# Performance work log

Hardware: AMD Instinct MI355X
Metric: run time of the kernel (lower is better)

## Reference

```python
import jax, jax.numpy as jnp
import numpy as np
from jax import lax

B, P, MAXDIM, RES = 128, 2048, 3, 4096
H = 1024          # hidden_dim
F = 256           # ph_feature_dim
H4 = H // 4       # 256
H2 = H // 2       # 512
LN_EPS = 1e-5


def setup_inputs() -> dict:
    key = jax.random.key(0)
    ks = jax.random.split(key, 16)
    inp = {
        "pd": jax.random.normal(ks[0], (B, P, 3), dtype=jnp.float32),
        "pd_lengths": jax.random.randint(ks[1], (B,), 0, P, dtype=jnp.int32),
        "betti_numbers": jax.random.randint(ks[2], (B, MAXDIM), 0, 12, dtype=jnp.int32),
        "persistence_images": jax.random.normal(ks[3], (B, RES), dtype=jnp.float32),
        # pd_encoder: Linear(3,F) -> LayerNorm(F) -> GELU -> Linear(F,H4)
        "W1": jax.random.normal(ks[4], (3, F), dtype=jnp.float32) * 0.1,
        "b1": jnp.zeros((F,), dtype=jnp.float32),
        "ln_g": jnp.ones((F,), dtype=jnp.float32),
        "ln_b": jnp.zeros((F,), dtype=jnp.float32),
        "W2": jax.random.normal(ks[5], (F, H4), dtype=jnp.float32) * 0.06,
        "b2": jnp.zeros((H4,), dtype=jnp.float32),
        # Embedding(10, H4)
        "betti_table": jax.random.normal(ks[6], (10, H4), dtype=jnp.float32),
        # Conv1d(1, H2, k=5, stride=2, pad=2)
        "conv_w": jax.random.normal(ks[7], (H2, 1, 5), dtype=jnp.float32) * 0.4,
        "conv_b": jnp.zeros((H2,), dtype=jnp.float32),
        # output_proj: Linear(H, H)
        "Wo": jax.random.normal(ks[8], (H, H), dtype=jnp.float32) * 0.03,
        "bo": jnp.zeros((H,), dtype=jnp.float32),
    }
    return inp


def reference(pd, pd_lengths, betti_numbers, persistence_images,
              W1, b1, ln_g, ln_b, W2, b2, betti_table, conv_w, conv_b, Wo, bo):
    dt = pd.dtype
    # --- PD branch: batched padded encode + masked mean pool ---
    mask = (jnp.arange(pd.shape[1])[None, :] < pd_lengths[:, None]).astype(dt)  # [B,P]
    h = jnp.einsum('bpi,if->bpf', pd, W1) + b1                                  # [B,P,F]
    mu = jnp.mean(h, axis=-1, keepdims=True)
    var = jnp.mean(jnp.square(h - mu), axis=-1, keepdims=True)                  # biased var (torch LN)
    h = (h - mu) * lax.rsqrt(var + LN_EPS) * ln_g + ln_b
    h = jax.nn.gelu(h, approximate=False)                                       # exact GELU (torch default)
    h = jnp.einsum('bpf,fd->bpd', h, W2) + b2                                   # [B,P,H4]
    counts = jnp.sum(mask, axis=1)                                              # [B]
    sums = jnp.einsum('bpd,bp->bd', h, mask)                                    # [B,H4]
    pd_pooled = jnp.where(counts[:, None] > 0, sums / jnp.maximum(counts, 1.0)[:, None], 0.0)
    # --- Betti branch: clamp -> embed -> mean over dims ---
    betti_feat = betti_table[jnp.clip(betti_numbers, 0, 9)].mean(axis=1)        # [B,H4]
    # --- Persistence-image branch: Conv1d(1,H2,k=5,s=2,p=2) then mean over positions ---
    pi = lax.conv_general_dilated(persistence_images[:, None, :], conv_w,
                                  window_strides=(2,), padding=[(2, 2)])        # [B,H2,L]
    pi_feat = pi.mean(axis=-1) + conv_b[None, :]                                # [B,H2]
    # --- Combine + output projection ---
    combined = jnp.concatenate([pd_pooled, betti_feat, pi_feat], axis=-1)       # [B,H]
    out = combined @ Wo + bo                                                    # [B,H]
    return out[:, None, :]                                                      # [B,1,H]
```

## Files before the change

kernel.cpp:

```cpp
#include <hip/hip_runtime.h>
#include <math.h>

constexpr int kB   = 128;
constexpr int kP   = 2048;
constexpr int kRES = 4096;
constexpr int kF   = 256;
constexpr int kH   = 1024;
constexpr float kLN_EPS = 1e-5f;
constexpr int kBN = 32;
constexpr int kBK = 64;
constexpr int kRSTD_BLOCKS = 512;

#if __has_builtin(__builtin_amdgcn_exp2f)
#define EXP2F __builtin_amdgcn_exp2f
#else
#define EXP2F exp2f
#endif
#if __has_builtin(__builtin_amdgcn_rcpf)
#define RCPF __builtin_amdgcn_rcpf
#else
#define RCPF(x) (1.0f / (x))
#endif

__device__ __forceinline__ float gelu_fast(float y) {
    const float a = fabsf(y);
    const float t = RCPF(fmaf(0.33267096f, a, 1.0f));
    const float e = EXP2F(-0.72134752f * y * y);
    const float p = fmaf(fmaf(0.37392780f, t, -0.04793990f), t, 0.17401210f);
    const float w = (p * t) * e;
    return fmaf(-a, w, fmaf(0.5f, y, 0.5f * a));
}

__device__ __forceinline__ void build_chain_starts(
    const int* __restrict__ plen, int C, int K, int tid,
    unsigned* s1, unsigned* s2, int* cs)
{
    if (tid < kB) s1[tid] = (unsigned)plen[tid] + (unsigned)K;
    __syncthreads();
    unsigned* src = s1; unsigned* dst = s2;
    #pragma unroll
    for (int d = 1; d < kB; d <<= 1) {
        if (tid < kB) dst[tid] = src[tid] + ((tid >= d) ? src[tid - d] : 0u);
        __syncthreads();
        unsigned* t = src; src = dst; dst = t;
    }
    const unsigned total = src[kB - 1];
    if (tid <= kB) {
        const unsigned pre = (tid == 0) ? 0u : src[tid - 1];
        cs[tid] = (int)(((unsigned long long)pre * (unsigned)C) / total);
    }
    __syncthreads();
}

__device__ __forceinline__ void ln_constants(
    const float* __restrict__ W1, const float* __restrict__ b1,
    int tid, float pr[14][4], float* cl)
{
    const float w0 = W1[tid], w1 = W1[256 + tid], w2 = W1[512 + tid], bb = b1[tid];
    float v[14] = { w0, w1, w2, bb, w0*w0, w0*w1, w0*w2, w1*w1, w1*w2, w2*w2,
                    w0*bb, w1*bb, w2*bb, bb*bb };
    #pragma unroll
    for (int off = 32; off; off >>= 1) {
        #pragma unroll
        for (int i = 0; i < 14; ++i) v[i] += __shfl_xor(v[i], off);
    }
    if ((tid & 63) == 0) {
        #pragma unroll
        for (int i = 0; i < 14; ++i) pr[i][tid >> 6] = v[i];
    }
    __syncthreads();
    if (tid < 14)
        cl[tid] = (pr[tid][0] + pr[tid][1] + pr[tid][2] + pr[tid][3]) * (1.f / 256.f);
    __syncthreads();
}

__global__ __launch_bounds__(256) void k0_setup(
    const int* __restrict__ plen, const float* __restrict__ W1,
    const float* __restrict__ b1, const float* __restrict__ ln_g,
    const float* __restrict__ pd,
    float* __restrict__ Wp, float* __restrict__ bp,
    int* __restrict__ cs_g, int4* __restrict__ ctab,
    float* __restrict__ rstdb, int C, int K)
{
    __shared__ unsigned s1[kB], s2[kB];
    __shared__ int cs[kB + 1];
    __shared__ float pr[14][4];
    __shared__ float cl[14];
    const int tid = threadIdx.x;
    const int bid = blockIdx.x;
    const int NB_TAB = C >> 8;

    if (bid >= NB_TAB) {
        ln_constants(W1, b1, tid, pr, cl);
        const float S0 = cl[0], S1c = cl[1], S2c = cl[2], Sb = cl[3];
        const float P00 = cl[4], P01 = cl[5], P02 = cl[6];
        const float P11 = cl[7], P12 = cl[8], P22 = cl[9];
        const float Q0 = cl[10], Q1 = cl[11], Q2 = cl[12], Rc = cl[13];
        const int rbase = (bid - NB_TAB) * 512;
        #pragma unroll
        for (int u = 0; u < 2; ++u) {
            const int r = rbase + u * 256 + tid;
            const float* rp = pd + (size_t)r * 3;
            const float x0 = rp[0], x1 = rp[1], x2 = rp[2];
            const float mu = fmaf(x2, S2c, fmaf(x1, S1c, fmaf(x0, S0, Sb)));
            const float sx = fmaf(P01 * x0, x1, fmaf(P02 * x0, x2, fmaf(P12 * x1, x2,
                             fmaf(Q0, x0, fmaf(Q1, x1, Q2 * x2)))));
            const float e2 = fmaf(P00 * x0, x0, fmaf(P11 * x1, x1, fmaf(P22 * x2, x2,
                             fmaf(2.f, sx, Rc))));
            rstdb[r] = rsqrtf(fmaf(-mu, mu, e2) + kLN_EPS);
        }
        return;
    }

    build_chain_starts(plen, C, K, tid, s1, s2, cs);

    const int c = bid * 256 + tid;
    {
        int lo = 0, hi = kB;
        while (hi - lo > 1) { const int mid = (lo + hi) >> 1; if (cs[mid] <= c) lo = mid; else hi = mid; }
        const int b = lo;
        const int m = cs[b + 1] - cs[b];
        const int j = c - cs[b];
        const int len = plen[b];
        const int T  = (len + 3) >> 2;
        const int l4 = (int)(((long long)j * T) / m);
        const int h4 = (int)(((long long)(j + 1) * T) / m);
        const int start = min(l4 * 4, len);
        const int cnt   = max(0, min(h4 * 4, len) - start);
        ctab[c] = make_int4(b, start, cnt, 0);
    }

    if (bid == 0) {
        if (tid <= kB) cs_g[tid] = cs[tid];
        ln_constants(W1, b1, tid, pr, cl);
        const float g = ln_g[tid];
        Wp[tid]       = (W1[tid]       - cl[0]) * g;
        Wp[256 + tid] = (W1[256 + tid] - cl[1]) * g;
        Wp[512 + tid] = (W1[512 + tid] - cl[2]) * g;
        bp[tid]       = (b1[tid]       - cl[3]) * g;
    }
}

__global__ __launch_bounds__(256) void k1_pd_partial(
    const float* __restrict__ pd, const float* __restrict__ Wp,
    const float* __restrict__ bp, const float* __restrict__ ln_b,
    const int4* __restrict__ ctab, const float* __restrict__ rstdb,
    float* __restrict__ partial)
{
    const int tid = threadIdx.x, lane = tid & 63, wave = tid >> 6;
    const int c = blockIdx.x * 4 + wave;
    const int4 ci = ctab[c];
    const int b = ci.x, start = ci.y, cnt = ci.z;

    const float4 w0q = ((const float4*)Wp)[lane];
    const float4 w1q = ((const float4*)Wp)[64 + lane];
    const float4 w2q = ((const float4*)Wp)[128 + lane];
    const float4 bpq = ((const float4*)bp)[lane];
    const float4 beq = ((const float4*)ln_b)[lane];

    float a0 = 0.f, a1 = 0.f, a2 = 0.f, a3 = 0.f;

#define ROW(x0, x1, x2, rs)                                                      \
    {                                                                            \
        const float h0 = fmaf((x2), w2q.x, fmaf((x1), w1q.x, fmaf((x0), w0q.x, bpq.x))); \
        const float h1 = fmaf((x2), w2q.y, fmaf((x1), w1q.y, fmaf((x0), w0q.y, bpq.y))); \
        const float h2 = fmaf((x2), w2q.z, fmaf((x1), w1q.z, fmaf((x0), w0q.z, bpq.z))); \
        const float h3 = fmaf((x2), w2q.w, fmaf((x1), w1q.w, fmaf((x0), w0q.w, bpq.w))); \
        a0 += gelu_fast(fmaf(h0, (rs), beq.x));                                  \
        a1 += gelu_fast(fmaf(h1, (rs), beq.y));                                  \
        a2 += gelu_fast(fmaf(h2, (rs), beq.z));                                  \
        a3 += gelu_fast(fmaf(h3, (rs), beq.w));                                  \
    }

    const int nq  = cnt >> 2;
    const int rem = cnt & 3;
    const float4* qp = (const float4*)(pd + ((size_t)b * kP + start) * 3);
    const float4* rs4 = (const float4*)(rstdb + (size_t)b * kP + start);
    for (int it = 0; it < nq; ++it) {
        const float4 f0 = qp[0];
        const float4 f1 = qp[1];
        const float4 f2 = qp[2];
        const float4 rq = rs4[it];
        qp += 3;
        ROW(f0.x, f0.y, f0.z, rq.x);
        ROW(f0.w, f1.x, f1.y, rq.y);
        ROW(f1.z, f1.w, f2.x, rq.z);
        ROW(f2.y, f2.z, f2.w, rq.w);
    }
    const float* rp = (const float*)qp;
    const float* rsp = rstdb + (size_t)b * kP + start + nq * 4;
    for (int it = 0; it < rem; ++it, rp += 3) {
        ROW(rp[0], rp[1], rp[2], rsp[it]);
    }
#undef ROW

    ((float4*)(partial + ((size_t)c << 8)))[lane] = make_float4(a0, a1, a2, a3);
}

__global__ __launch_bounds__(256) void k2_combined(
    const float* __restrict__ partial, const int* __restrict__ plen,
    const float* __restrict__ W2, const float* __restrict__ b2,
    const int* __restrict__ betti, const float* __restrict__ betti_table,
    const float* __restrict__ pimg, const float* __restrict__ conv_w,
    const float* __restrict__ conv_b, float* __restrict__ combined,
    const int* __restrict__ cs_g)
{
    __shared__ float red[4 * 256];
    __shared__ float ml[256];
    __shared__ float sred[2][4];
    const int b    = blockIdx.x;
    const int tid  = threadIdx.x;
    const int wave = tid >> 6;
    const int lane = tid & 63;

    if (blockIdx.y == 0) {
        const int len = plen[b];
        const int c0 = cs_g[b], c1 = cs_g[b + 1];

        float4 aq = make_float4(0.f, 0.f, 0.f, 0.f);
        float4 bq = make_float4(0.f, 0.f, 0.f, 0.f);
        int c = c0 + wave;
        for (; c + 4 < c1; c += 8) {
            const float4 v0 = ((const float4*)(partial + ((size_t)c << 8)))[lane];
            const float4 v1 = ((const float4*)(partial + ((size_t)(c + 4) << 8)))[lane];
            aq.x += v0.x; aq.y += v0.y; aq.z += v0.z; aq.w += v0.w;
            bq.x += v1.x; bq.y += v1.y; bq.z += v1.z; bq.w += v1.w;
        }
        if (c < c1) {
            const float4 v0 = ((const float4*)(partial + ((size_t)c << 8)))[lane];
            aq.x += v0.x; aq.y += v0.y; aq.z += v0.z; aq.w += v0.w;
        }
        aq.x += bq.x; aq.y += bq.y; aq.z += bq.z; aq.w += bq.w;
        ((float4*)red)[wave * 64 + lane] = aq;
        __syncthreads();
        const float inv = (len > 0) ? (1.f / (float)len) : 0.f;
        ml[tid] = (red[tid] + red[256 + tid] + red[512 + tid] + red[768 + tid]) * inv;
        __syncthreads();

        const float4* W24 = (const float4*)W2;
        float4 acc = make_float4(0.f, 0.f, 0.f, 0.f);
        const int f0 = wave * 64;
        #pragma unroll 8
        for (int i = 0; i < 64; ++i) {
            const float mv = ml[f0 + i];
            const float4 wv = W24[(size_t)(f0 + i) * 64 + lane];
            acc.x = fmaf(mv, wv.x, acc.x); acc.y = fmaf(mv, wv.y, acc.y);
            acc.z = fmaf(mv, wv.z, acc.z); acc.w = fmaf(mv, wv.w, acc.w);
        }
        ((float4*)red)[wave * 64 + lane] = acc;
        __syncthreads();
        const float o = (red[tid] + red[256 + tid]) + (red[512 + tid] + red[768 + tid]);
        combined[(size_t)b * kH + tid] = (len > 0) ? (o + b2[tid]) : 0.f;

        const int i0 = min(max(betti[b * 3 + 0], 0), 9);
        const int i1 = min(max(betti[b * 3 + 1], 0), 9);
        const int i2 = min(max(betti[b * 3 + 2], 0), 9);
        combined[(size_t)b * kH + 256 + tid] =
            (betti_table[i0 * 256 + tid] + betti_table[i1 * 256 + tid] +
             betti_table[i2 * 256 + tid]) * (1.f / 3.f);
    } else {
        const float4* x4 = (const float4*)(pimg + (size_t)b * kRES);
        float se = 0.f, so = 0.f;
        #pragma unroll
        for (int j = 0; j < 4; ++j) {
            const float4 v = x4[tid + j * 256];
            se += v.x + v.z;
            so += v.y + v.w;
        }
        #pragma unroll
        for (int off = 32; off; off >>= 1) {
            se += __shfl_xor(se, off);
            so += __shfl_xor(so, off);
        }
        if (lane == 0) { sred[0][wave] = se; sred[1][wave] = so; }
        __syncthreads();
        se = (sred[0][0] + sred[0][1]) + (sred[0][2] + sred[0][3]);
        so = (sred[1][0] + sred[1][1]) + (sred[1][2] + sred[1][3]);

        const float x0 = pimg[(size_t)b * kRES + 0];
        const float xe = pimg[(size_t)b * kRES + 4094];
        const float xo = pimg[(size_t)b * kRES + 4095];
        #pragma unroll
        for (int u = 0; u < 2; ++u) {
            const int cc = tid + u * 256;
            const float* w = conv_w + (size_t)cc * 5;
            const float v = w[0] * (se - xe) + w[1] * (so - xo) + w[2] * se +
                            w[3] * so + w[4] * (se - x0);
            combined[(size_t)b * kH + 512 + cc] = v * (1.f / 2048.f) + conv_b[cc];
        }
    }
}

__global__ __launch_bounds__(256) void k3a_outproj(
    const float* __restrict__ combined, const float* __restrict__ Wo,
    float* __restrict__ kpart, int KT)
{
    const int nt  = blockIdx.x;
    const int kt  = blockIdx.y;
    const int tid = threadIdx.x;
    const int n0  = nt * kBN;
    const int kchunk = kH / KT;
    const int nsub   = kchunk / kBK;

    __shared__ float At[kBK * 132];
    __shared__ float Bs[kBK * kBN];

    const int n8 = tid & 7;
    const int mg = tid >> 3;

    float4 acc0 = make_float4(0.f,0.f,0.f,0.f);
    float4 acc1 = make_float4(0.f,0.f,0.f,0.f);
    float4 acc2 = make_float4(0.f,0.f,0.f,0.f);
    float4 acc3 = make_float4(0.f,0.f,0.f,0.f);

    for (int sc = 0; sc < nsub; ++sc) {
        const int k0 = kt * kchunk + sc * kBK;
        __syncthreads();
        #pragma unroll
        for (int it = 0; it < 8; ++it) {
            const int idx = it * 256 + tid;
            const int m   = idx >> 4;
            const int c4  = idx & 15;
            const float4 v = *(const float4*)(combined + (size_t)m * kH + k0 + c4 * 4);
            At[(c4 * 4 + 0) * 132 + m] = v.x;
            At[(c4 * 4 + 1) * 132 + m] = v.y;
            At[(c4 * 4 + 2) * 132 + m] = v.z;
            At[(c4 * 4 + 3) * 132 + m] = v.w;
        }
        #pragma unroll
        for (int it = 0; it < 2; ++it) {
            const int idx = it * 256 + tid;
            const int kk  = idx >> 3;
            const int cc  = idx & 7;
            *(float4*)(Bs + kk * kBN + cc * 4) =
                *(const float4*)(Wo + (size_t)(k0 + kk) * kH + n0 + cc * 4);
        }
        __syncthreads();

        #pragma unroll 8
        for (int kk = 0; kk < kBK; ++kk) {
            const float4 av = *(const float4*)(At + kk * 132 + mg * 4);
            const float4 bv = *(const float4*)(Bs + kk * kBN + n8 * 4);
            acc0.x = fmaf(av.x, bv.x, acc0.x); acc0.y = fmaf(av.x, bv.y, acc0.y);
            acc0.z = fmaf(av.x, bv.z, acc0.z); acc0.w = fmaf(av.x, bv.w, acc0.w);
            acc1.x = fmaf(av.y, bv.x, acc1.x); acc1.y = fmaf(av.y, bv.y, acc1.y);
            acc1.z = fmaf(av.y, bv.z, acc1.z); acc1.w = fmaf(av.y, bv.w, acc1.w);
            acc2.x = fmaf(av.z, bv.x, acc2.x); acc2.y = fmaf(av.z, bv.y, acc2.y);
            acc2.z = fmaf(av.z, bv.z, acc2.z); acc2.w = fmaf(av.z, bv.w, acc2.w);
            acc3.x = fmaf(av.w, bv.x, acc3.x); acc3.y = fmaf(av.w, bv.y, acc3.y);
            acc3.z = fmaf(av.w, bv.z, acc3.z); acc3.w = fmaf(av.w, bv.w, acc3.w);
        }
    }

    float* base = kpart + ((size_t)kt * kB + mg * 4) * kH + n0 + n8 * 4;
    *(float4*)(base)          = acc0;
    *(float4*)(base + kH)     = acc1;
    *(float4*)(base + 2 * kH) = acc2;
    *(float4*)(base + 3 * kH) = acc3;
}

__global__ __launch_bounds__(256) void k3b_reduce(
    const float* __restrict__ kpart, const float* __restrict__ bo,
    float* __restrict__ out, int KT)
{
    const int g = blockIdx.x * 256 + threadIdx.x;
    const float4* kp = (const float4*)kpart;
    float4 a = make_float4(0.f, 0.f, 0.f, 0.f);
    float4 b = make_float4(0.f, 0.f, 0.f, 0.f);
    float4 cacc = make_float4(0.f, 0.f, 0.f, 0.f);
    float4 d = make_float4(0.f, 0.f, 0.f, 0.f);
    int t = 0;
    for (; t + 3 < KT; t += 4) {
        const float4 v0 = kp[(size_t)(t + 0) * (kB * kH / 4) + g];
        const float4 v1 = kp[(size_t)(t + 1) * (kB * kH / 4) + g];
        const float4 v2 = kp[(size_t)(t + 2) * (kB * kH / 4) + g];
        const float4 v3 = kp[(size_t)(t + 3) * (kB * kH / 4) + g];
        a.x += v0.x; a.y += v0.y; a.z += v0.z; a.w += v0.w;
        b.x += v1.x; b.y += v1.y; b.z += v1.z; b.w += v1.w;
        cacc.x += v2.x; cacc.y += v2.y; cacc.z += v2.z; cacc.w += v2.w;
        d.x += v3.x; d.y += v3.y; d.z += v3.z; d.w += v3.w;
    }
    for (; t < KT; ++t) {
        const float4 v0 = kp[(size_t)t * (kB * kH / 4) + g];
        a.x += v0.x; a.y += v0.y; a.z += v0.z; a.w += v0.w;
    }
    a.x += b.x + cacc.x + d.x;
    a.y += b.y + cacc.y + d.y;
    a.z += b.z + cacc.z + d.z;
    a.w += b.w + cacc.w + d.w;
    const float4 bq = ((const float4*)bo)[g & 255];
    a.x += bq.x; a.y += bq.y; a.z += bq.z; a.w += bq.w;
    ((float4*)out)[g] = a;
}

extern "C" void kernel_launch(void* const* d_in, const int* in_sizes, int n_in,
                              void* d_out, int out_size, void* d_ws, size_t ws_size,
                              hipStream_t stream) {
    const float* pd   = (const float*)d_in[0];
    const int*   plen = (const int*)  d_in[1];
    const int*   bnum = (const int*)  d_in[2];
    const float* pimg = (const float*)d_in[3];
    const float* W1   = (const float*)d_in[4];
    const float* b1   = (const float*)d_in[5];
    const float* lng  = (const float*)d_in[6];
    const float* lnb  = (const float*)d_in[7];
    const float* W2   = (const float*)d_in[8];
    const float* b2   = (const float*)d_in[9];
    const float* btab = (const float*)d_in[10];
    const float* cw   = (const float*)d_in[11];
    const float* cb   = (const float*)d_in[12];
    const float* Wo   = (const float*)d_in[13];
    const float* bo   = (const float*)d_in[14];
    float* out = (float*)d_out;

    int C = 2048;
    {
        const int Cs[3] = {8192, 4096, 2048};
        for (int i = 0; i < 3; ++i) {
            const size_t need = ((size_t)Cs[i] * 256 + (size_t)kB * kH + 768 + 256 + 132) * 4 +
                                (size_t)Cs[i] * 16 + (size_t)kB * kP * 4 + 256;
            if (ws_size >= need) { C = Cs[i]; break; }
        }
    }
    const int K  = (kB * kP + C - 129) / (C - 128);
    const int KT = C / 512;

    float* partial  = (float*)d_ws;
    float* combined = partial + (size_t)C * 256;
    float* Wp       = combined + (size_t)kB * kH;
    float* bpp      = Wp + 768;
    int*   cs_g     = (int*)(bpp + 256);
    int4*  ctab     = (int4*)(cs_g + 132);
    float* rstdb    = (float*)(ctab + C);
    float* kpart    = partial;

    k0_setup<<<dim3(C / 256 + kRSTD_BLOCKS), 256, 0, stream>>>(
        plen, W1, b1, lng, pd, Wp, bpp, cs_g, ctab, rstdb, C, K);
    k1_pd_partial<<<dim3(C / 4), 256, 0, stream>>>(pd, Wp, bpp, lnb, ctab, rstdb, partial);
    k2_combined<<<dim3(kB, 2), 256, 0, stream>>>(partial, plen, W2, b2, bnum, btab,
                                                 pimg, cw, cb, combined, cs_g);
    k3a_outproj<<<dim3(32, KT), 256, 0, stream>>>(combined, Wo, kpart, KT);
    k3b_reduce<<<dim3(kB), 256, 0, stream>>>(kpart, bo, out, KT);
}
```

Baseline: 52.38 us.

## Fuse setup kernel into PD partial kernel, recomputing chunk table and rstd inline

Removes the separate k0_setup launch. Every k1 block now recomputes the LayerNorm constants, chain starts and its chunk assignment, and each wave computes per-row rstd into shared memory instead of reading a precomputed global buffer. k2 also rebuilds the chain starts locally. This saves a launch plus the rstd and table round trips through global memory, at the cost of redundant per-block setup work (reductions and syncs) in every k1 and k2 block.

```diff
diff --git a/kernel.cpp b/kernel.cpp
--- a/kernel.cpp
+++ b/kernel.cpp
@@ -9,7 +9,6 @@
 constexpr float kLN_EPS = 1e-5f;
 constexpr int kBN = 32;
 constexpr int kBK = 64;
-constexpr int kRSTD_BLOCKS = 512;
 
 #if __has_builtin(__builtin_amdgcn_exp2f)
 #define EXP2F __builtin_amdgcn_exp2f
@@ -74,89 +73,54 @@
     __syncthreads();
 }
 
-__global__ __launch_bounds__(256) void k0_setup(
-    const int* __restrict__ plen, const float* __restrict__ W1,
-    const float* __restrict__ b1, const float* __restrict__ ln_g,
-    const float* __restrict__ pd,
-    float* __restrict__ Wp, float* __restrict__ bp,
-    int* __restrict__ cs_g, int4* __restrict__ ctab,
-    float* __restrict__ rstdb, int C, int K)
+__global__ __launch_bounds__(256) void k1_pd_partial(
+    const float* __restrict__ pd, const int* __restrict__ plen,
+    const float* __restrict__ W1, const float* __restrict__ b1,
+    const float* __restrict__ ln_g, const float* __restrict__ ln_b,
+    float* __restrict__ partial, int C, int K)
 {
     __shared__ unsigned s1[kB], s2[kB];
     __shared__ int cs[kB + 1];
     __shared__ float pr[14][4];
     __shared__ float cl[14];
-    const int tid = threadIdx.x;
-    const int bid = blockIdx.x;
-    const int NB_TAB = C >> 8;
-
-    if (bid >= NB_TAB) {
-        ln_constants(W1, b1, tid, pr, cl);
-        const float S0 = cl[0], S1c = cl[1], S2c = cl[2], Sb = cl[3];
-        const float P00 = cl[4], P01 = cl[5], P02 = cl[6];
-        const float P11 = cl[7], P12 = cl[8], P22 = cl[9];
-        const float Q0 = cl[10], Q1 = cl[11], Q2 = cl[12], Rc = cl[13];
-        const int rbase = (bid - NB_TAB) * 512;
-        #pragma unroll
-        for (int u = 0; u < 2; ++u) {
-            const int r = rbase + u * 256 + tid;
-            const float* rp = pd + (size_t)r * 3;
-            const float x0 = rp[0], x1 = rp[1], x2 = rp[2];
-            const float mu = fmaf(x2, S2c, fmaf(x1, S1c, fmaf(x0, S0, Sb)));
-            const float sx = fmaf(P01 * x0, x1, fmaf(P02 * x0, x2, fmaf(P12 * x1, x2,
-                             fmaf(Q0, x0, fmaf(Q1, x1, Q2 * x2)))));
-            const float e2 = fmaf(P00 * x0, x0, fmaf(P11 * x1, x1, fmaf(P22 * x2, x2,
-                             fmaf(2.f, sx, Rc))));
-            rstdb[r] = rsqrtf(fmaf(-mu, mu, e2) + kLN_EPS);
-        }
-        return;
-    }
-
+    __shared__ float rstd_s[4][64];
+    const int tid = threadIdx.x, lane = tid & 63, wave = tid >> 6;
+
+    ln_constants(W1, b1, tid, pr, cl);
     build_chain_starts(plen, C, K, tid, s1, s2, cs);
 
-    const int c = bid * 256 + tid;
-    {
-        int lo = 0, hi = kB;
-        while (hi - lo > 1) { const int mid = (lo + hi) >> 1; if (cs[mid] <= c) lo = mid; else hi = mid; }
-        const int b = lo;
-        const int m = cs[b + 1] - cs[b];
-        const int j = c - cs[b];
-        const int len = plen[b];
-        const int T  = (len + 3) >> 2;
-        const int l4 = (int)(((long long)j * T) / m);
-        const int h4 = (int)(((long long)(j + 1) * T) / m);
-        const int start = min(l4 * 4, len);
-        const int cnt   = max(0, min(h4 * 4, len) - start);
-        ctab[c] = make_int4(b, start, cnt, 0);
-    }
-
-    if (bid == 0) {
-        if (tid <= kB) cs_g[tid] = cs[tid];
-        ln_constants(W1, b1, tid, pr, cl);
-        const float g = ln_g[tid];
-        Wp[tid]       = (W1[tid]       - cl[0]) * g;
-        Wp[256 + tid] = (W1[256 + tid] - cl[1]) * g;
-        Wp[512 + tid] = (W1[512 + tid] - cl[2]) * g;
-        bp[tid]       = (b1[tid]       - cl[3]) * g;
-    }
-}
-
-__global__ __launch_bounds__(256) void k1_pd_partial(
-    const float* __restrict__ pd, const float* __restrict__ Wp,
-    const float* __restrict__ bp, const float* __restrict__ ln_b,
-    const int4* __restrict__ ctab, const float* __restrict__ rstdb,
-    float* __restrict__ partial)
-{
-    const int tid = threadIdx.x, lane = tid & 63, wave = tid >> 6;
+    const float S0 = cl[0], S1c = cl[1], S2c = cl[2], Sb = cl[3];
+    const float P00 = cl[4], P01 = cl[5], P02 = cl[6];
+    const float P11 = cl[7], P12 = cl[8], P22 = cl[9];
+    const float Q0 = cl[10], Q1 = cl[11], Q2 = cl[12], Rc = cl[13];
+
     const int c = blockIdx.x * 4 + wave;
-    const int4 ci = ctab[c];
-    const int b = ci.x, start = ci.y, cnt = ci.z;
-
-    const float4 w0q = ((const float4*)Wp)[lane];
-    const float4 w1q = ((const float4*)Wp)[64 + lane];
-    const float4 w2q = ((const float4*)Wp)[128 + lane];
-    const float4 bpq = ((const float4*)bp)[lane];
+    int lo = 0, hi = kB;
+    while (hi - lo > 1) { const int mid = (lo + hi) >> 1; if (cs[mid] <= c) lo = mid; else hi = mid; }
+    const int b = lo;
+    const int m = cs[b + 1] - cs[b];
+    const int j = c - cs[b];
+    const int len = plen[b];
+    const int T  = (len + 3) >> 2;
+    const int l4 = (int)(((long long)j * T) / m);
+    const int h4 = (int)(((long long)(j + 1) * T) / m);
+    const int start = min(l4 * 4, len);
+    const int cnt   = max(0, min(h4 * 4, len) - start);
+
+    const float4 W04 = ((const float4*)W1)[lane];
+    const float4 W14 = ((const float4*)W1)[64 + lane];
+    const float4 W24 = ((const float4*)W1)[128 + lane];
+    const float4 B14 = ((const float4*)b1)[lane];
+    const float4 G4  = ((const float4*)ln_g)[lane];
     const float4 beq = ((const float4*)ln_b)[lane];
+    const float4 w0q = make_float4((W04.x - S0) * G4.x, (W04.y - S0) * G4.y,
+                                   (W04.z - S0) * G4.z, (W04.w - S0) * G4.w);
+    const float4 w1q = make_float4((W14.x - S1c) * G4.x, (W14.y - S1c) * G4.y,
+                                   (W14.z - S1c) * G4.z, (W14.w - S1c) * G4.w);
+    const float4 w2q = make_float4((W24.x - S2c) * G4.x, (W24.y - S2c) * G4.y,
+                                   (W24.z - S2c) * G4.z, (W24.w - S2c) * G4.w);
+    const float4 bpq = make_float4((B14.x - Sb) * G4.x, (B14.y - Sb) * G4.y,
+                                   (B14.z - Sb) * G4.z, (B14.w - Sb) * G4.w);
 
     float a0 = 0.f, a1 = 0.f, a2 = 0.f, a3 = 0.f;
 
@@ -172,25 +136,39 @@
         a3 += gelu_fast(fmaf(h3, (rs), beq.w));                                  \
     }
 
-    const int nq  = cnt >> 2;
-    const int rem = cnt & 3;
-    const float4* qp = (const float4*)(pd + ((size_t)b * kP + start) * 3);
-    const float4* rs4 = (const float4*)(rstdb + (size_t)b * kP + start);
-    for (int it = 0; it < nq; ++it) {
-        const float4 f0 = qp[0];
-        const float4 f1 = qp[1];
-        const float4 f2 = qp[2];
-        const float4 rq = rs4[it];
-        qp += 3;
-        ROW(f0.x, f0.y, f0.z, rq.x);
-        ROW(f0.w, f1.x, f1.y, rq.y);
-        ROW(f1.z, f1.w, f2.x, rq.z);
-        ROW(f2.y, f2.z, f2.w, rq.w);
-    }
-    const float* rp = (const float*)qp;
-    const float* rsp = rstdb + (size_t)b * kP + start + nq * 4;
-    for (int it = 0; it < rem; ++it, rp += 3) {
-        ROW(rp[0], rp[1], rp[2], rsp[it]);
+    for (int off = 0; off < cnt; off += 64) {
+        const int n = min(64, cnt - off);
+        {
+            const int rr = start + off + ((lane < n) ? lane : 0);
+            const float* rp = pd + ((size_t)b * kP + rr) * 3;
+            const float x0 = rp[0], x1 = rp[1], x2 = rp[2];
+            const float mu = fmaf(x2, S2c, fmaf(x1, S1c, fmaf(x0, S0, Sb)));
+            const float sx = fmaf(P01 * x0, x1, fmaf(P02 * x0, x2, fmaf(P12 * x1, x2,
+                             fmaf(Q0, x0, fmaf(Q1, x1, Q2 * x2)))));
+            const float e2 = fmaf(P00 * x0, x0, fmaf(P11 * x1, x1, fmaf(P22 * x2, x2,
+                             fmaf(2.f, sx, Rc))));
+            rstd_s[wave][lane] = rsqrtf(fmaf(-mu, mu, e2) + kLN_EPS);
+        }
+        const int nq  = n >> 2;
+        const int rem = n & 3;
+        const float4* qp = (const float4*)(pd + ((size_t)b * kP + start + off) * 3);
+        for (int q = 0; q < nq; ++q) {
+            const float4 f0 = qp[0];
+            const float4 f1 = qp[1];
+            const float4 f2 = qp[2];
+            const float4 rq = *(const float4*)&rstd_s[wave][q * 4];
+            qp += 3;
+            ROW(f0.x, f0.y, f0.z, rq.x);
+            ROW(f0.w, f1.x, f1.y, rq.y);
+            ROW(f1.z, f1.w, f2.x, rq.z);
+            ROW(f2.y, f2.z, f2.w, rq.w);
+        }
+        if (rem) {
+            const float* rp = (const float*)qp;
+            for (int i = 0; i < rem; ++i, rp += 3) {
+                ROW(rp[0], rp[1], rp[2], rstd_s[wave][nq * 4 + i]);
+            }
+        }
     }
 #undef ROW
 
@@ -203,8 +181,10 @@
     const int* __restrict__ betti, const float* __restrict__ betti_table,
     const float* __restrict__ pimg, const float* __restrict__ conv_w,
     const float* __restrict__ conv_b, float* __restrict__ combined,
-    const int* __restrict__ cs_g)
-{
+    int C, int K)
+{
+    __shared__ unsigned s1[kB], s2[kB];
+    __shared__ int cs[kB + 1];
     __shared__ float red[4 * 256];
     __shared__ float ml[256];
     __shared__ float sred[2][4];
@@ -214,8 +194,9 @@
     const int lane = tid & 63;
 
     if (blockIdx.y == 0) {
+        build_chain_starts(plen, C, K, tid, s1, s2, cs);
         const int len = plen[b];
-        const int c0 = cs_g[b], c1 = cs_g[b + 1];
+        const int c0 = cs[b], c1 = cs[b + 1];
 
         float4 aq = make_float4(0.f, 0.f, 0.f, 0.f);
         float4 bq = make_float4(0.f, 0.f, 0.f, 0.f);
@@ -417,8 +398,7 @@
     {
         const int Cs[3] = {8192, 4096, 2048};
         for (int i = 0; i < 3; ++i) {
-            const size_t need = ((size_t)Cs[i] * 256 + (size_t)kB * kH + 768 + 256 + 132) * 4 +
-                                (size_t)Cs[i] * 16 + (size_t)kB * kP * 4 + 256;
+            const size_t need = ((size_t)Cs[i] * 256 + (size_t)kB * kH) * 4;
             if (ws_size >= need) { C = Cs[i]; break; }
         }
     }
@@ -427,18 +407,12 @@
 
     float* partial  = (float*)d_ws;
     float* combined = partial + (size_t)C * 256;
-    float* Wp       = combined + (size_t)kB * kH;
-    float* bpp      = Wp + 768;
-    int*   cs_g     = (int*)(bpp + 256);
-    int4*  ctab     = (int4*)(cs_g + 132);
-    float* rstdb    = (float*)(ctab + C);
     float* kpart    = partial;
 
-    k0_setup<<<dim3(C / 256 + kRSTD_BLOCKS), 256, 0, stream>>>(
-        plen, W1, b1, lng, pd, Wp, bpp, cs_g, ctab, rstdb, C, K);
-    k1_pd_partial<<<dim3(C / 4), 256, 0, stream>>>(pd, Wp, bpp, lnb, ctab, rstdb, partial);
+    k1_pd_partial<<<dim3(C / 4), 256, 0, stream>>>(pd, plen, W1, b1, lng, lnb,
+                                                   partial, C, K);
     k2_combined<<<dim3(kB, 2), 256, 0, stream>>>(partial, plen, W2, b2, bnum, btab,
-                                                 pimg, cw, cb, combined, cs_g);
+                                                 pimg, cw, cb, combined, C, K);
     k3a_outproj<<<dim3(32, KT), 256, 0, stream>>>(combined, Wo, kpart, KT);
     k3b_reduce<<<dim3(kB), 256, 0, stream>>>(kpart, bo, out, KT);
 }
```

Measured after the change: 53.71 us. 1.03x slower.

## Fuse output-projection split-K reduction into GEMM via atomic ticket counter

Applied to the files above, without the earlier changes.

Merges the split-K output projection and its reduction kernel into one launch. Each block takes an atomic ticket after writing its partial tile. The last 32 ticket holders spin until every block has finished, then each sums the partials for 4 output row groups and adds the bias. This removes one kernel launch and its gap, at the cost of a memset, a spin-wait that relies on all blocks being co-resident or already retired, and the reduction now running on only 32 blocks instead of 128.

```diff
diff --git a/kernel.cpp b/kernel.cpp
--- a/kernel.cpp
+++ b/kernel.cpp
@@ -291,9 +291,10 @@
     }
 }
 
-__global__ __launch_bounds__(256) void k3a_outproj(
+__global__ __launch_bounds__(256) void k3_fused(
     const float* __restrict__ combined, const float* __restrict__ Wo,
-    float* __restrict__ kpart, int KT)
+    float* __restrict__ kpart, const float* __restrict__ bo,
+    float* __restrict__ out, int* __restrict__ cnt3, int KT)
 {
     const int nt  = blockIdx.x;
     const int kt  = blockIdx.y;
@@ -304,6 +305,7 @@
 
     __shared__ float At[kBK * 132];
     __shared__ float Bs[kBK * kBN];
+    __shared__ int s_ticket;
 
     const int n8 = tid & 7;
     const int mg = tid >> 3;
@@ -357,40 +359,56 @@
     *(float4*)(base + kH)     = acc1;
     *(float4*)(base + 2 * kH) = acc2;
     *(float4*)(base + 3 * kH) = acc3;
-}
-
-__global__ __launch_bounds__(256) void k3b_reduce(
-    const float* __restrict__ kpart, const float* __restrict__ bo,
-    float* __restrict__ out, int KT)
-{
-    const int g = blockIdx.x * 256 + threadIdx.x;
+
+    __syncthreads();
+    if (tid == 0) {
+        __threadfence();
+        s_ticket = atomicAdd(cnt3, 1);
+    }
+    __syncthreads();
+    const int NB3 = 32 * KT;
+    const int ticket = s_ticket;
+    if (ticket < NB3 - 32) return;
+
+    if (tid == 0) {
+        while (__hip_atomic_load(cnt3, __ATOMIC_ACQUIRE, __HIP_MEMORY_SCOPE_AGENT) < NB3)
+            __builtin_amdgcn_s_sleep(8);
+    }
+    __syncthreads();
+    __threadfence();
+
     const float4* kp = (const float4*)kpart;
-    float4 a = make_float4(0.f, 0.f, 0.f, 0.f);
-    float4 b = make_float4(0.f, 0.f, 0.f, 0.f);
-    float4 cacc = make_float4(0.f, 0.f, 0.f, 0.f);
-    float4 d = make_float4(0.f, 0.f, 0.f, 0.f);
-    int t = 0;
-    for (; t + 3 < KT; t += 4) {
-        const float4 v0 = kp[(size_t)(t + 0) * (kB * kH / 4) + g];
-        const float4 v1 = kp[(size_t)(t + 1) * (kB * kH / 4) + g];
-        const float4 v2 = kp[(size_t)(t + 2) * (kB * kH / 4) + g];
-        const float4 v3 = kp[(size_t)(t + 3) * (kB * kH / 4) + g];
-        a.x += v0.x; a.y += v0.y; a.z += v0.z; a.w += v0.w;
-        b.x += v1.x; b.y += v1.y; b.z += v1.z; b.w += v1.w;
-        cacc.x += v2.x; cacc.y += v2.y; cacc.z += v2.z; cacc.w += v2.w;
-        d.x += v3.x; d.y += v3.y; d.z += v3.z; d.w += v3.w;
-    }
-    for (; t < KT; ++t) {
-        const float4 v0 = kp[(size_t)t * (kB * kH / 4) + g];
-        a.x += v0.x; a.y += v0.y; a.z += v0.z; a.w += v0.w;
-    }
-    a.x += b.x + cacc.x + d.x;
-    a.y += b.y + cacc.y + d.y;
-    a.z += b.z + cacc.z + d.z;
-    a.w += b.w + cacc.w + d.w;
-    const float4 bq = ((const float4*)bo)[g & 255];
-    a.x += bq.x; a.y += bq.y; a.z += bq.z; a.w += bq.w;
-    ((float4*)out)[g] = a;
+    const int base_gb = (ticket - (NB3 - 32)) * 4;
+    #pragma unroll
+    for (int i = 0; i < 4; ++i) {
+        const int g = (base_gb + i) * 256 + tid;
+        float4 a = make_float4(0.f, 0.f, 0.f, 0.f);
+        float4 b = make_float4(0.f, 0.f, 0.f, 0.f);
+        float4 cc = make_float4(0.f, 0.f, 0.f, 0.f);
+        float4 d = make_float4(0.f, 0.f, 0.f, 0.f);
+        int t = 0;
+        for (; t + 3 < KT; t += 4) {
+            const float4 v0 = kp[(size_t)(t + 0) * (kB * kH / 4) + g];
+            const float4 v1 = kp[(size_t)(t + 1) * (kB * kH / 4) + g];
+            const float4 v2 = kp[(size_t)(t + 2) * (kB * kH / 4) + g];
+            const float4 v3 = kp[(size_t)(t + 3) * (kB * kH / 4) + g];
+            a.x += v0.x; a.y += v0.y; a.z += v0.z; a.w += v0.w;
+            b.x += v1.x; b.y += v1.y; b.z += v1.z; b.w += v1.w;
+            cc.x += v2.x; cc.y += v2.y; cc.z += v2.z; cc.w += v2.w;
+            d.x += v3.x; d.y += v3.y; d.z += v3.z; d.w += v3.w;
+        }
+        for (; t < KT; ++t) {
+            const float4 v0 = kp[(size_t)t * (kB * kH / 4) + g];
+            a.x += v0.x; a.y += v0.y; a.z += v0.z; a.w += v0.w;
+        }
+        a.x += b.x + cc.x + d.x;
+        a.y += b.y + cc.y + d.y;
+        a.z += b.z + cc.z + d.z;
+        a.w += b.w + cc.w + d.w;
+        const float4 bq = ((const float4*)bo)[g & 255];
+        a.x += bq.x; a.y += bq.y; a.z += bq.z; a.w += bq.w;
+        ((float4*)out)[g] = a;
+    }
 }
 
 extern "C" void kernel_launch(void* const* d_in, const int* in_sizes, int n_in,
@@ -432,13 +450,14 @@
     int*   cs_g     = (int*)(bpp + 256);
     int4*  ctab     = (int4*)(cs_g + 132);
     float* rstdb    = (float*)(ctab + C);
+    int*   cnts     = (int*)(rstdb + (size_t)kB * kP);
     float* kpart    = partial;
 
+    hipMemsetAsync(cnts, 0, 64, stream);
     k0_setup<<<dim3(C / 256 + kRSTD_BLOCKS), 256, 0, stream>>>(
         plen, W1, b1, lng, pd, Wp, bpp, cs_g, ctab, rstdb, C, K);
     k1_pd_partial<<<dim3(C / 4), 256, 0, stream>>>(pd, Wp, bpp, lnb, ctab, rstdb, partial);
     k2_combined<<<dim3(kB, 2), 256, 0, stream>>>(partial, plen, W2, b2, bnum, btab,
                                                  pimg, cw, cb, combined, cs_g);
-    k3a_outproj<<<dim3(32, KT), 256, 0, stream>>>(combined, Wo, kpart, KT);
-    k3b_reduce<<<dim3(kB), 256, 0, stream>>>(kpart, bo, out, KT);
-}
+    k3_fused<<<dim3(32, KT), 256, 0, stream>>>(combined, Wo, kpart, bo, out, cnts, KT);
+}
```

Measured after the change: 88.47 us. 68.9% more time.

## Replace split-K partial buffer and reduce kernel with atomic accumulation into output

Applied to the files above, without the earlier changes.

The output projection's split-K partials are now accumulated directly into the output with float atomicAdd, which removes the separate reduce kernel and its partial-buffer round trip. The output is first initialised with the bias inside the combined-features kernel. The chunk-count choice also drops its largest option, which lowers the split-K factor and so the number of atomic contributions per element. In exchange, 16 scalar atomics per thread may contend, and the summation order becomes nondeterministic.

```diff
diff --git a/kernel.cpp b/kernel.cpp
--- a/kernel.cpp
+++ b/kernel.cpp
@@ -113,7 +113,6 @@
     }
 
     build_chain_starts(plen, C, K, tid, s1, s2, cs);
-
     const int c = bid * 256 + tid;
     {
         int lo = 0, hi = kB;
@@ -129,7 +128,6 @@
         const int cnt   = max(0, min(h4 * 4, len) - start);
         ctab[c] = make_int4(b, start, cnt, 0);
     }
-
     if (bid == 0) {
         if (tid <= kB) cs_g[tid] = cs[tid];
         ln_constants(W1, b1, tid, pr, cl);
@@ -203,7 +201,8 @@
     const int* __restrict__ betti, const float* __restrict__ betti_table,
     const float* __restrict__ pimg, const float* __restrict__ conv_w,
     const float* __restrict__ conv_b, float* __restrict__ combined,
-    const int* __restrict__ cs_g)
+    const int* __restrict__ cs_g, const float* __restrict__ bo,
+    float* __restrict__ out)
 {
     __shared__ float red[4 * 256];
     __shared__ float ml[256];
@@ -212,6 +211,11 @@
     const int tid  = threadIdx.x;
     const int wave = tid >> 6;
     const int lane = tid & 63;
+
+    if (tid < 128) {
+        const int f4 = blockIdx.y * 128 + tid;
+        ((float4*)(out + (size_t)b * kH))[f4] = ((const float4*)bo)[f4];
+    }
 
     if (blockIdx.y == 0) {
         const int len = plen[b];
@@ -291,9 +295,9 @@
     }
 }
 
-__global__ __launch_bounds__(256) void k3a_outproj(
+__global__ __launch_bounds__(256) void k3_atomic(
     const float* __restrict__ combined, const float* __restrict__ Wo,
-    float* __restrict__ kpart, int KT)
+    float* __restrict__ out, int KT)
 {
     const int nt  = blockIdx.x;
     const int kt  = blockIdx.y;
@@ -352,45 +356,15 @@
         }
     }
 
-    float* base = kpart + ((size_t)kt * kB + mg * 4) * kH + n0 + n8 * 4;
-    *(float4*)(base)          = acc0;
-    *(float4*)(base + kH)     = acc1;
-    *(float4*)(base + 2 * kH) = acc2;
-    *(float4*)(base + 3 * kH) = acc3;
-}
-
-__global__ __launch_bounds__(256) void k3b_reduce(
-    const float* __restrict__ kpart, const float* __restrict__ bo,
-    float* __restrict__ out, int KT)
-{
-    const int g = blockIdx.x * 256 + threadIdx.x;
-    const float4* kp = (const float4*)kpart;
-    float4 a = make_float4(0.f, 0.f, 0.f, 0.f);
-    float4 b = make_float4(0.f, 0.f, 0.f, 0.f);
-    float4 cacc = make_float4(0.f, 0.f, 0.f, 0.f);
-    float4 d = make_float4(0.f, 0.f, 0.f, 0.f);
-    int t = 0;
-    for (; t + 3 < KT; t += 4) {
-        const float4 v0 = kp[(size_t)(t + 0) * (kB * kH / 4) + g];
-        const float4 v1 = kp[(size_t)(t + 1) * (kB * kH / 4) + g];
-        const float4 v2 = kp[(size_t)(t + 2) * (kB * kH / 4) + g];
-        const float4 v3 = kp[(size_t)(t + 3) * (kB * kH / 4) + g];
-        a.x += v0.x; a.y += v0.y; a.z += v0.z; a.w += v0.w;
-        b.x += v1.x; b.y += v1.y; b.z += v1.z; b.w += v1.w;
-        cacc.x += v2.x; cacc.y += v2.y; cacc.z += v2.z; cacc.w += v2.w;
-        d.x += v3.x; d.y += v3.y; d.z += v3.z; d.w += v3.w;
-    }
-    for (; t < KT; ++t) {
-        const float4 v0 = kp[(size_t)t * (kB * kH / 4) + g];
-        a.x += v0.x; a.y += v0.y; a.z += v0.z; a.w += v0.w;
-    }
-    a.x += b.x + cacc.x + d.x;
-    a.y += b.y + cacc.y + d.y;
-    a.z += b.z + cacc.z + d.z;
-    a.w += b.w + cacc.w + d.w;
-    const float4 bq = ((const float4*)bo)[g & 255];
-    a.x += bq.x; a.y += bq.y; a.z += bq.z; a.w += bq.w;
-    ((float4*)out)[g] = a;
+    float* base = out + ((size_t)mg * 4) * kH + n0 + n8 * 4;
+    atomicAdd(base + 0,          acc0.x); atomicAdd(base + 1,          acc0.y);
+    atomicAdd(base + 2,          acc0.z); atomicAdd(base + 3,          acc0.w);
+    atomicAdd(base + kH + 0,     acc1.x); atomicAdd(base + kH + 1,     acc1.y);
+    atomicAdd(base + kH + 2,     acc1.z); atomicAdd(base + kH + 3,     acc1.w);
+    atomicAdd(base + 2*kH + 0,   acc2.x); atomicAdd(base + 2*kH + 1,   acc2.y);
+    atomicAdd(base + 2*kH + 2,   acc2.z); atomicAdd(base + 2*kH + 3,   acc2.w);
+    atomicAdd(base + 3*kH + 0,   acc3.x); atomicAdd(base + 3*kH + 1,   acc3.y);
+    atomicAdd(base + 3*kH + 2,   acc3.z); atomicAdd(base + 3*kH + 3,   acc3.w);
 }
 
 extern "C" void kernel_launch(void* const* d_in, const int* in_sizes, int n_in,
@@ -415,8 +389,8 @@
 
     int C = 2048;
     {
-        const int Cs[3] = {8192, 4096, 2048};
-        for (int i = 0; i < 3; ++i) {
+        const int Cs[2] = {4096, 2048};
+        for (int i = 0; i < 2; ++i) {
             const size_t need = ((size_t)Cs[i] * 256 + (size_t)kB * kH + 768 + 256 + 132) * 4 +
                                 (size_t)Cs[i] * 16 + (size_t)kB * kP * 4 + 256;
             if (ws_size >= need) { C = Cs[i]; break; }
@@ -432,13 +406,11 @@
     int*   cs_g     = (int*)(bpp + 256);
     int4*  ctab     = (int4*)(cs_g + 132);
     float* rstdb    = (float*)(ctab + C);
-    float* kpart    = partial;
 
     k0_setup<<<dim3(C / 256 + kRSTD_BLOCKS), 256, 0, stream>>>(
         plen, W1, b1, lng, pd, Wp, bpp, cs_g, ctab, rstdb, C, K);
     k1_pd_partial<<<dim3(C / 4), 256, 0, stream>>>(pd, Wp, bpp, lnb, ctab, rstdb, partial);
     k2_combined<<<dim3(kB, 2), 256, 0, stream>>>(partial, plen, W2, b2, bnum, btab,
-                                                 pimg, cw, cb, combined, cs_g);
-    k3a_outproj<<<dim3(32, KT), 256, 0, stream>>>(combined, Wo, kpart, KT);
-    k3b_reduce<<<dim3(kB), 256, 0, stream>>>(kpart, bo, out, KT);
-}
+                                                 pimg, cw, cb, combined, cs_g, bo, out);
+    k3_atomic<<<dim3(32, KT), 256, 0, stream>>>(combined, Wo, out, KT);
+}
```

Measured after the change: 58.32 us. 1.11x slower.
